# Kernel optimization log

Hardware: AMD Instinct MI355X
Metric: run time of the kernel (lower is better)

## Reference

```python
import jax, jax.numpy as jnp
import numpy as np

GROUP_SIZES = np.array([64, 48, 56, 40, 32, 24, 16, 8])
N_GROUPS = 8
MAX_GS = 64
D_MODEL = 2048
BATCH = 8192


def setup_inputs() -> dict:
    key = jax.random.key(0)
    k1, k2, k3, k4 = jax.random.split(key, 4)
    hidden = jax.random.normal(k1, (BATCH, N_GROUPS, D_MODEL), dtype=jnp.float32)
    chosen = jax.random.randint(k2, (BATCH,), 0, N_GROUPS)
    scale = 1.0 / np.sqrt(D_MODEL)  # nn.Linear default init range
    W = jax.random.uniform(k3, (N_GROUPS, MAX_GS, D_MODEL), minval=-scale, maxval=scale, dtype=jnp.float32)
    b = jax.random.uniform(k4, (N_GROUPS, MAX_GS), minval=-scale, maxval=scale, dtype=jnp.float32)
    gs = jnp.asarray(GROUP_SIZES, dtype=jnp.int32)
    # zero-pad decoder rows beyond each group's true output size
    row_mask = jnp.arange(MAX_GS)[None, :] < gs[:, None]  # [G, MAX_GS]
    W = W * row_mask[:, :, None]
    b = b * row_mask
    return {"hidden": hidden, "chosen_group_idx": chosen, "W": W, "b": b, "group_sizes": gs}


def reference(hidden, chosen_group_idx, W, b, group_sizes):
    # hidden: [B, G, D]; chosen_group_idx: [B]; W: [G, MAX_GS, D] (zero-padded); b: [G, MAX_GS]
    # Gather each sample's chosen group slice: [B, D]
    h = jnp.take_along_axis(hidden, chosen_group_idx[:, None, None], axis=1)[:, 0, :]
    Wg = W[chosen_group_idx]  # [B, MAX_GS, D]
    bg = b[chosen_group_idx]  # [B, MAX_GS]
    preds = jnp.einsum('bd,bgd->bg', h, Wg) + bg  # [B, MAX_GS]
    valid = jnp.arange(W.shape[1])[None, :] < group_sizes[chosen_group_idx][:, None]
    preds = jnp.where(valid, preds, 0.0)  # padded slots are zero, as in the torch module
    return preds, valid
```

## Files before the change

kernel.cpp:

```cpp
#include <hip/hip_runtime.h>
#include <hip/hip_bf16.h>

#define BATCH   8192
#define NGRP    8
#define MAXGS   64
#define DMODEL  2048
#define TM      16
#define NBLK    32
#define NKK     (DMODEL / 32)
#define KC      512
#define NCH     (DMODEL / KC)
#define KKP     (KC / 32)
#define MAXTILES 520

typedef __attribute__((ext_vector_type(8))) short  short8;
typedef __attribute__((ext_vector_type(4))) float  f32x4;

#define CNT_OFF   0
#define HIST_OFF  512
#define MAP_OFF   1536
#define LISTS_OFF 4096
#define W_OFF     (LISTS_OFF + NGRP * BATCH * 4)
#define CNT_STRIDE 16

static __device__ __forceinline__ short bf(float f) {
    __hip_bfloat16 h = __float2bfloat16(f);
    return (short)__bfloat16_as_ushort(h);
}

__global__ __launch_bounds__(256) void init_hist_kernel(
    const float* __restrict__ W,
    const int* __restrict__ chosen,
    unsigned short* __restrict__ Wb2,
    int* __restrict__ hist)
{
    int blk = blockIdx.x;
    int tid = threadIdx.x;
    if (blk < 1024) {
        int e = (blk * 256 + tid) * 4;
        int g = e >> 17;
        int rem = e & ((MAXGS * DMODEL) - 1);
        int c = rem >> 11;
        int k = rem & (DMODEL - 1);
        int kk = k >> 5, j = k & 31;
        float4 w = *reinterpret_cast<const float4*>(W + e);
        ushort4 o;
        o.x = (unsigned short)bf(w.x); o.y = (unsigned short)bf(w.y);
        o.z = (unsigned short)bf(w.z); o.w = (unsigned short)bf(w.w);
        size_t dst = (((size_t)g * NKK + kk) * MAXGS + c) * 32 + j;
        *reinterpret_cast<ushort4*>(Wb2 + dst) = o;
    } else {
        int hb = blk - 1024;
        __shared__ int h[NGRP];
        if (tid < NGRP) h[tid] = 0;
        __syncthreads();
        int g = chosen[hb * 256 + tid];
        atomicAdd(&h[g], 1);
        __syncthreads();
        if (tid < NGRP) hist[hb * NGRP + tid] = h[tid];
    }
}

__global__ __launch_bounds__(256) void scatter_kernel(const int* __restrict__ chosen,
                                                      const int* __restrict__ hist,
                                                      int* __restrict__ lists,
                                                      int* __restrict__ cnt,
                                                      int* __restrict__ map) {
    __shared__ int hloc[NBLK * NGRP];
    __shared__ int gbase[NGRP];
    __shared__ int ntl[NGRP];
    __shared__ int wcnt[4][NGRP];
    __shared__ int wbase[4][NGRP];
    int tid  = threadIdx.x;
    int blk  = blockIdx.x;
    int w    = tid >> 6;
    int lane = tid & 63;

    if (tid < NBLK * NGRP) hloc[tid] = hist[tid];
    __syncthreads();
    if (tid < NGRP) {
        int s = 0;
        for (int b2 = 0; b2 < blk; ++b2) s += hloc[b2 * NGRP + tid];
        gbase[tid] = s;
        int tot = s;
        for (int b2 = blk; b2 < NBLK; ++b2) tot += hloc[b2 * NGRP + tid];
        ntl[tid] = (tot + TM - 1) / TM;
        if (blk == 0) cnt[tid * CNT_STRIDE] = tot;
    }
    __syncthreads();

    if (blk == 0) {
        for (int q = tid; q < MAXTILES; q += 256) map[q] = -1;
        __syncthreads();
        for (int p = tid; p < NGRP * 512; p += 256) {
            int t = p >> 3, gg = p & 7;
            if (t < ntl[gg]) {
                int pos = 0;
                #pragma unroll
                for (int g2 = 0; g2 < NGRP; ++g2) {
                    int nt = ntl[g2];
                    pos += (t < nt ? t : nt);
                    pos += (g2 < gg && nt > t) ? 1 : 0;
                }
                map[pos] = (gg << 16) | t;
            }
        }
    }

    int b = blk * 256 + tid;
    int g = chosen[b];
    int rank = 0;
    unsigned long long below = (1ull << lane) - 1ull;
    #pragma unroll
    for (int gg = 0; gg < NGRP; ++gg) {
        unsigned long long m = __ballot(g == gg);
        if (g == gg) rank = __popcll(m & below);
        if (lane == gg) wcnt[w][gg] = __popcll(m);
    }
    __syncthreads();
    if (tid < NGRP) {
        int base = gbase[tid];
        #pragma unroll
        for (int ww = 0; ww < 4; ++ww) {
            wbase[ww][tid] = base;
            base += wcnt[ww][tid];
        }
    }
    __syncthreads();
    lists[g * BATCH + wbase[w][g] + rank] = b;
}

__global__ __launch_bounds__(256, 4) void gemm_kernel(
    const float* __restrict__ hidden,
    const float* __restrict__ bias,
    const int* __restrict__ gsizes,
    const int* __restrict__ cnt,
    const int* __restrict__ lists,
    const int* __restrict__ map,
    const unsigned short* __restrict__ Wb2,
    float* __restrict__ out)
{
    int e = map[blockIdx.x];
    if (e < 0) return;
    int g = e >> 16;
    int t = e & 0xFFFF;
    int c = cnt[g * CNT_STRIDE];
    int m0 = t * TM;

    __shared__ unsigned short A[2][TM][KC];

    int tid  = threadIdx.x;
    int w    = tid >> 6;
    int lane = tid & 63;
    int lrow = lane & 15;
    int kg   = lane >> 4;

    const float* src[4];
    #pragma unroll
    for (int i = 0; i < 4; ++i) {
        int m  = m0 + 4 * w + i;
        int ms = m < c ? m : c - 1;
        src[i] = hidden + ((size_t)lists[g * BATCH + ms] * NGRP + g) * DMODEL
               + lane * 8;
    }

    auto STAGE = [&](int buf, int ch) {
        f32x4 v0[4], v1[4];
        #pragma unroll
        for (int i = 0; i < 4; ++i) {
            v0[i] = *reinterpret_cast<const f32x4*>(src[i] + ch * KC);
            v1[i] = *reinterpret_cast<const f32x4*>(src[i] + ch * KC + 4);
        }
        #pragma unroll
        for (int i = 0; i < 4; ++i) {
            int r = 4 * w + i;
            int swz = ((r & 3) << 4) | (((r >> 3) & 1) << 6);
            short8 o;
            o[0] = bf(v0[i][0]); o[1] = bf(v0[i][1]);
            o[2] = bf(v0[i][2]); o[3] = bf(v0[i][3]);
            o[4] = bf(v1[i][0]); o[5] = bf(v1[i][1]);
            o[6] = bf(v1[i][2]); o[7] = bf(v1[i][3]);
            char* ab = (char*)&A[buf][r][0];
            *reinterpret_cast<short8*>(ab + ((lane * 16) ^ swz)) = o;
        }
    };

    int swzr = ((lrow & 3) << 4) | (((lrow >> 3) & 1) << 6);
    const unsigned short* bp =
        Wb2 + (size_t)g * NKK * MAXGS * 32 + (w * 16 + lrow) * 32 + kg * 8;
    f32x4 acc = f32x4{0, 0, 0, 0};

    STAGE(0, 0);
    __syncthreads();
    #pragma unroll
    for (int ch = 0; ch < NCH; ++ch) {
        if (ch + 1 < NCH) STAGE((ch + 1) & 1, ch + 1);
        const char* abase = (const char*)&A[ch & 1][lrow][0];
        #pragma unroll 8
        for (int k2 = 0; k2 < KKP; ++k2) {
            int byte = (k2 * 64 + kg * 16) ^ swzr;
            short8 af  = *reinterpret_cast<const short8*>(abase + byte);
            short8 bfr = *reinterpret_cast<const short8*>(
                bp + (size_t)(ch * KKP + k2) * MAXGS * 32);
            acc = __builtin_amdgcn_mfma_f32_16x16x32_bf16(af, bfr, acc, 0, 0, 0);
        }
        __syncthreads();
    }

    int gsz = gsizes[g];
    int n = w * 16 + lrow;
    float bv = bias[g * MAXGS + n];
    #pragma unroll
    for (int r = 0; r < 4; ++r) {
        int m = m0 + kg * 4 + r;
        if (m < c) {
            int s = lists[g * BATCH + m];
            out[(size_t)s * MAXGS + n] = acc[r] + bv;
            out[(size_t)(BATCH + s) * MAXGS + n] = (n < gsz) ? 1.0f : 0.0f;
        }
    }
}

extern "C" void kernel_launch(void* const* d_in, const int* in_sizes, int n_in,
                              void* d_out, int out_size, void* d_ws, size_t ws_size,
                              hipStream_t stream) {
    const float* hidden = (const float*)d_in[0];
    const int*   chosen = (const int*)d_in[1];
    const float* W      = (const float*)d_in[2];
    const float* bias   = (const float*)d_in[3];
    const int*   gs     = (const int*)d_in[4];
    float* out = (float*)d_out;

    char* ws = (char*)d_ws;
    int* cnt   = (int*)(ws + CNT_OFF);
    int* hist  = (int*)(ws + HIST_OFF);
    int* map   = (int*)(ws + MAP_OFF);
    int* lists = (int*)(ws + LISTS_OFF);
    unsigned short* Wb2 = (unsigned short*)(ws + W_OFF);

    init_hist_kernel<<<dim3(1024 + NBLK), dim3(256), 0, stream>>>(W, chosen, Wb2, hist);
    scatter_kernel<<<dim3(NBLK), dim3(256), 0, stream>>>(chosen, hist, lists, cnt, map);
    gemm_kernel<<<dim3(MAXTILES), dim3(256), 0, stream>>>(
        hidden, bias, gs, cnt, lists, map, Wb2, out);
}
```

Baseline: 37.36 us.

## Drop separate W bf16 conversion pass; convert W tiles in-GEMM via shared memory

Removes the pre-pass that converted and relaid the full weight tensor to bf16 in workspace. Each GEMM block now loads fp32 W rows for its group directly, converts them to bf16 and stages them in swizzled LDS alongside the A tile, with KC halved to 256 and global loads issued before the MFMA loop and LDS writes after it. This saves a 4MB read plus 2MB write pass and one launch's worth of work. In exchange every tile re-reads 512KB of fp32 W (mostly from L2), which raises register pressure and lowers occupancy (launch bound changes from 4 to 2 blocks).

```diff
diff --git a/kernel.cpp b/kernel.cpp
--- a/kernel.cpp
+++ b/kernel.cpp
@@ -7,8 +7,7 @@
 #define DMODEL  2048
 #define TM      16
 #define NBLK    32
-#define NKK     (DMODEL / 32)
-#define KC      512
+#define KC      256
 #define NCH     (DMODEL / KC)
 #define KKP     (KC / 32)
 #define MAXTILES 520
@@ -20,7 +19,6 @@
 #define HIST_OFF  512
 #define MAP_OFF   1536
 #define LISTS_OFF 4096
-#define W_OFF     (LISTS_OFF + NGRP * BATCH * 4)
 #define CNT_STRIDE 16
 
 static __device__ __forceinline__ short bf(float f) {
@@ -28,37 +26,16 @@
     return (short)__bfloat16_as_ushort(h);
 }
 
-__global__ __launch_bounds__(256) void init_hist_kernel(
-    const float* __restrict__ W,
-    const int* __restrict__ chosen,
-    unsigned short* __restrict__ Wb2,
-    int* __restrict__ hist)
-{
-    int blk = blockIdx.x;
+__global__ __launch_bounds__(256) void hist_kernel(const int* __restrict__ chosen,
+                                                   int* __restrict__ hist) {
     int tid = threadIdx.x;
-    if (blk < 1024) {
-        int e = (blk * 256 + tid) * 4;
-        int g = e >> 17;
-        int rem = e & ((MAXGS * DMODEL) - 1);
-        int c = rem >> 11;
-        int k = rem & (DMODEL - 1);
-        int kk = k >> 5, j = k & 31;
-        float4 w = *reinterpret_cast<const float4*>(W + e);
-        ushort4 o;
-        o.x = (unsigned short)bf(w.x); o.y = (unsigned short)bf(w.y);
-        o.z = (unsigned short)bf(w.z); o.w = (unsigned short)bf(w.w);
-        size_t dst = (((size_t)g * NKK + kk) * MAXGS + c) * 32 + j;
-        *reinterpret_cast<ushort4*>(Wb2 + dst) = o;
-    } else {
-        int hb = blk - 1024;
-        __shared__ int h[NGRP];
-        if (tid < NGRP) h[tid] = 0;
-        __syncthreads();
-        int g = chosen[hb * 256 + tid];
-        atomicAdd(&h[g], 1);
-        __syncthreads();
-        if (tid < NGRP) hist[hb * NGRP + tid] = h[tid];
-    }
+    __shared__ int h[NGRP];
+    if (tid < NGRP) h[tid] = 0;
+    __syncthreads();
+    int g = chosen[blockIdx.x * 256 + tid];
+    atomicAdd(&h[g], 1);
+    __syncthreads();
+    if (tid < NGRP) hist[blockIdx.x * NGRP + tid] = h[tid];
 }
 
 __global__ __launch_bounds__(256) void scatter_kernel(const int* __restrict__ chosen,
@@ -130,14 +107,14 @@
     lists[g * BATCH + wbase[w][g] + rank] = b;
 }
 
-__global__ __launch_bounds__(256, 4) void gemm_kernel(
+__global__ __launch_bounds__(256, 2) void gemm_kernel(
     const float* __restrict__ hidden,
+    const float* __restrict__ W,
     const float* __restrict__ bias,
     const int* __restrict__ gsizes,
     const int* __restrict__ cnt,
     const int* __restrict__ lists,
     const int* __restrict__ map,
-    const unsigned short* __restrict__ Wb2,
     float* __restrict__ out)
 {
     int e = map[blockIdx.x];
@@ -147,7 +124,8 @@
     int c = cnt[g * CNT_STRIDE];
     int m0 = t * TM;
 
-    __shared__ unsigned short A[2][TM][KC];
+    __shared__ unsigned short As[2][TM][KC];
+    __shared__ unsigned short Bs[2][MAXGS][KC];
 
     int tid  = threadIdx.x;
     int w    = tid >> 6;
@@ -155,60 +133,79 @@
     int lrow = lane & 15;
     int kg   = lane >> 4;
 
-    const float* src[4];
-    #pragma unroll
-    for (int i = 0; i < 4; ++i) {
-        int m  = m0 + 4 * w + i;
-        int ms = m < c ? m : c - 1;
-        src[i] = hidden + ((size_t)lists[g * BATCH + ms] * NGRP + g) * DMODEL
-               + lane * 8;
-    }
-
-    auto STAGE = [&](int buf, int ch) {
-        f32x4 v0[4], v1[4];
-        #pragma unroll
-        for (int i = 0; i < 4; ++i) {
-            v0[i] = *reinterpret_cast<const f32x4*>(src[i] + ch * KC);
-            v1[i] = *reinterpret_cast<const f32x4*>(src[i] + ch * KC + 4);
-        }
-        #pragma unroll
-        for (int i = 0; i < 4; ++i) {
-            int r = 4 * w + i;
-            int swz = ((r & 3) << 4) | (((r >> 3) & 1) << 6);
+    int arow = 4 * w + kg;
+    int am   = m0 + arow;
+    int ams  = am < c ? am : c - 1;
+    const float* asrc = hidden + ((size_t)lists[g * BATCH + ams] * NGRP + g) * DMODEL
+                      + lrow * 16;
+    int bcol = 16 * w + lrow;
+    const float* bsrc = W + ((size_t)g * MAXGS + bcol) * DMODEL + kg * 64;
+
+    int swzA_w = ((arow & 3) << 4) | (((arow >> 3) & 1) << 6);
+    int swzB_w = ((bcol & 3) << 4) | (((bcol >> 2) & 1) << 6);
+    int swzA_r = ((lrow & 3) << 4) | (((lrow >> 3) & 1) << 6);
+    int swzB_r = ((lrow & 3) << 4) | (((lrow >> 2) & 1) << 6);
+    f32x4 ar[4];
+    f32x4 br[16];
+
+    auto LOAD = [&](int ch) {
+        #pragma unroll
+        for (int j = 0; j < 4; ++j)
+            ar[j] = *reinterpret_cast<const f32x4*>(asrc + ch * KC + j * 4);
+        #pragma unroll
+        for (int j = 0; j < 16; ++j)
+            br[j] = *reinterpret_cast<const f32x4*>(bsrc + ch * KC + j * 4);
+    };
+    auto WRITE = [&](int buf) {
+        char* ab = (char*)&As[buf][arow][0];
+        #pragma unroll
+        for (int j2 = 0; j2 < 2; ++j2) {
             short8 o;
-            o[0] = bf(v0[i][0]); o[1] = bf(v0[i][1]);
-            o[2] = bf(v0[i][2]); o[3] = bf(v0[i][3]);
-            o[4] = bf(v1[i][0]); o[5] = bf(v1[i][1]);
-            o[6] = bf(v1[i][2]); o[7] = bf(v1[i][3]);
-            char* ab = (char*)&A[buf][r][0];
-            *reinterpret_cast<short8*>(ab + ((lane * 16) ^ swz)) = o;
+            #pragma unroll
+            for (int q2 = 0; q2 < 2; ++q2) {
+                f32x4 v = ar[j2 * 2 + q2];
+                o[q2*4+0] = bf(v[0]); o[q2*4+1] = bf(v[1]);
+                o[q2*4+2] = bf(v[2]); o[q2*4+3] = bf(v[3]);
+            }
+            *reinterpret_cast<short8*>(ab + ((lrow * 32 + j2 * 16) ^ swzA_w)) = o;
+        }
+        char* bb = (char*)&Bs[buf][bcol][0];
+        #pragma unroll
+        for (int i = 0; i < 8; ++i) {
+            short8 o;
+            #pragma unroll
+            for (int q2 = 0; q2 < 2; ++q2) {
+                f32x4 v = br[i * 2 + q2];
+                o[q2*4+0] = bf(v[0]); o[q2*4+1] = bf(v[1]);
+                o[q2*4+2] = bf(v[2]); o[q2*4+3] = bf(v[3]);
+            }
+            *reinterpret_cast<short8*>(bb + ((kg * 128 + i * 16) ^ swzB_w)) = o;
         }
     };
 
-    int swzr = ((lrow & 3) << 4) | (((lrow >> 3) & 1) << 6);
-    const unsigned short* bp =
-        Wb2 + (size_t)g * NKK * MAXGS * 32 + (w * 16 + lrow) * 32 + kg * 8;
     f32x4 acc = f32x4{0, 0, 0, 0};
 
-    STAGE(0, 0);
+    LOAD(0);
+    WRITE(0);
     __syncthreads();
     #pragma unroll
     for (int ch = 0; ch < NCH; ++ch) {
-        if (ch + 1 < NCH) STAGE((ch + 1) & 1, ch + 1);
-        const char* abase = (const char*)&A[ch & 1][lrow][0];
-        #pragma unroll 8
+        if (ch + 1 < NCH) LOAD(ch + 1);
+        const char* abase = (const char*)&As[ch & 1][lrow][0];
+        const char* bbase = (const char*)&Bs[ch & 1][bcol][0];
+        #pragma unroll
         for (int k2 = 0; k2 < KKP; ++k2) {
-            int byte = (k2 * 64 + kg * 16) ^ swzr;
-            short8 af  = *reinterpret_cast<const short8*>(abase + byte);
-            short8 bfr = *reinterpret_cast<const short8*>(
-                bp + (size_t)(ch * KKP + k2) * MAXGS * 32);
+            int kb = k2 * 64 + kg * 16;
+            short8 af  = *reinterpret_cast<const short8*>(abase + (kb ^ swzA_r));
+            short8 bfr = *reinterpret_cast<const short8*>(bbase + (kb ^ swzB_r));
             acc = __builtin_amdgcn_mfma_f32_16x16x32_bf16(af, bfr, acc, 0, 0, 0);
         }
+        if (ch + 1 < NCH) WRITE((ch + 1) & 1);
         __syncthreads();
     }
 
     int gsz = gsizes[g];
-    int n = w * 16 + lrow;
+    int n = 16 * w + lrow;
     float bv = bias[g * MAXGS + n];
     #pragma unroll
     for (int r = 0; r < 4; ++r) {
@@ -236,10 +233,9 @@
     int* hist  = (int*)(ws + HIST_OFF);
     int* map   = (int*)(ws + MAP_OFF);
     int* lists = (int*)(ws + LISTS_OFF);
-    unsigned short* Wb2 = (unsigned short*)(ws + W_OFF);
-
-    init_hist_kernel<<<dim3(1024 + NBLK), dim3(256), 0, stream>>>(W, chosen, Wb2, hist);
+
+    hist_kernel<<<dim3(NBLK), dim3(256), 0, stream>>>(chosen, hist);
     scatter_kernel<<<dim3(NBLK), dim3(256), 0, stream>>>(chosen, hist, lists, cnt, map);
     gemm_kernel<<<dim3(MAXTILES), dim3(256), 0, stream>>>(
-        hidden, bias, gs, cnt, lists, map, Wb2, out);
-}
+        hidden, W, bias, gs, cnt, lists, map, out);
+}
```

After: 72.01 us. 1.93x slower.
